# Performance work log

Measured on AMD Instinct MI355X. Metric: run time of the kernel, lower is better.

Reference implementation:

```python
import jax, jax.numpy as jnp
import numpy as np

EPS = 1e-12  # F.normalize default eps


def setup_inputs() -> dict:
    key = jax.random.key(0)
    k1, k2, k3, k4 = jax.random.split(key, 4)
    dim, heads = 192, 6
    B, H, W = 8, 128, 128
    x = jax.random.normal(k1, (B, dim, H, W), dtype=jnp.float32)
    qkv_w = jax.random.normal(k2, (3 * dim, dim), dtype=jnp.float32) * 0.05
    qkv_dw_w = jax.random.normal(k3, (3 * dim, 1, 3, 3), dtype=jnp.float32) * 0.05
    proj_w = jax.random.normal(k4, (dim, dim), dtype=jnp.float32) * 0.05
    temperature = jnp.ones((heads, 1, 1), dtype=jnp.float32)
    return {"x": x, "qkv_w": qkv_w, "qkv_dw_w": qkv_dw_w,
            "proj_w": proj_w, "temperature": temperature}


def _l2norm(t):
    # F.normalize(t, dim=-1): t / max(||t||_2, eps)
    n = jnp.sqrt(jnp.sum(t * t, axis=-1, keepdims=True))
    return t / jnp.maximum(n, EPS)


def reference(x, qkv_w, qkv_dw_w, proj_w, temperature):
    B, C, H, W = x.shape
    heads = temperature.shape[0]
    ch = C // heads  # channels per head

    # 1x1 pointwise conv (no bias)
    qkv = jnp.einsum('oc,bchw->bohw', qkv_w, x)
    # depthwise 3x3 conv, padding=1, groups = 3*C
    qkv = jax.lax.conv_general_dilated(
        qkv, qkv_dw_w, window_strides=(1, 1), padding='SAME',
        feature_group_count=3 * C,
        dimension_numbers=('NCHW', 'OIHW', 'NCHW'))

    q, k, v = jnp.split(qkv, 3, axis=1)
    # b (hd c) h w -> b hd c (h w)
    def split_heads(t):
        return t.reshape(B, heads, ch, H * W)
    q, k, v = split_heads(q), split_heads(k), split_heads(v)

    q = _l2norm(q)
    k = _l2norm(k)

    # channel attention: [b, hd, c, c], contraction over HW
    attn = jnp.einsum('bhcn,bhdn->bhcd', q, k) * temperature[None]
    attn = jax.nn.softmax(attn, axis=-1)

    out = jnp.einsum('bhcd,bhdn->bhcn', attn, v)  # [b, hd, c, HW]
    out = out.reshape(B, C, H, W)
    # final 1x1 projection
    return jnp.einsum('oc,bchw->bohw', proj_w, out)
```

## Files before the change

### kernel.cpp

```cpp
#include <hip/hip_runtime.h>
#include <type_traits>

typedef __attribute__((ext_vector_type(8))) short bf16x8;
typedef __attribute__((ext_vector_type(4))) float f32x4;

#define NB 8
#define NC 192
#define NO 576
#define NHW 16384
#define NH 6

__device__ __forceinline__ float bf2f(unsigned short u){
  return __uint_as_float(((unsigned int)u) << 16);
}
__device__ __forceinline__ unsigned short f2bf(float f){
  unsigned int u = __float_as_uint(f);
  u += 0x7FFFu + ((u >> 16) & 1u);
  return (unsigned short)(u >> 16);
}

__device__ __forceinline__ void st1(unsigned short* p, float v){ *p = f2bf(v); }
__device__ __forceinline__ void st1(float* p, float v){ *p = v; }

#define LSTR 200

__global__ void cvt_w(const float* __restrict__ w, unsigned short* __restrict__ wb, int n4){
  const int i = blockIdx.x*256 + threadIdx.x;
  if (i < n4){
    float4 f = *(const float4*)(w + (long long)i*4);
    *(ushort4*)(wb + (long long)i*4) = make_ushort4(f2bf(f.x), f2bf(f.y), f2bf(f.z), f2bf(f.w));
  }
}

template<typename BT, typename OT>
__global__ __launch_bounds__(256) void gemm192v2(
    const unsigned short* __restrict__ A, long long a_bstride, int o_tiles,
    const BT* __restrict__ Bm, long long b_bstride,
    OT* __restrict__ Out, long long o_bstride)
{
  __shared__ __align__(16) unsigned short Xt[128 * LSTR];
  const int t  = threadIdx.x;
  const int b  = blockIdx.z;
  const int n0 = blockIdx.x * 128;
  const BT* Bb = Bm + b_bstride * b;

  for (int idx = t; idx < 1536; idx += 256){
    const int n4 = (idx & 31) * 4;
    const int c  = (idx >> 5) * 4;
    if constexpr (std::is_same<BT, float>::value){
      float4 f0 = *(const float4*)(Bb + (long long)(c+0)*NHW + n0 + n4);
      float4 f1 = *(const float4*)(Bb + (long long)(c+1)*NHW + n0 + n4);
      float4 f2 = *(const float4*)(Bb + (long long)(c+2)*NHW + n0 + n4);
      float4 f3 = *(const float4*)(Bb + (long long)(c+3)*NHW + n0 + n4);
      *(ushort4*)&Xt[(n4+0)*LSTR + c] = make_ushort4(f2bf(f0.x), f2bf(f1.x), f2bf(f2.x), f2bf(f3.x));
      *(ushort4*)&Xt[(n4+1)*LSTR + c] = make_ushort4(f2bf(f0.y), f2bf(f1.y), f2bf(f2.y), f2bf(f3.y));
      *(ushort4*)&Xt[(n4+2)*LSTR + c] = make_ushort4(f2bf(f0.z), f2bf(f1.z), f2bf(f2.z), f2bf(f3.z));
      *(ushort4*)&Xt[(n4+3)*LSTR + c] = make_ushort4(f2bf(f0.w), f2bf(f1.w), f2bf(f2.w), f2bf(f3.w));
    } else {
      ushort4 u0 = *(const ushort4*)(Bb + (long long)(c+0)*NHW + n0 + n4);
      ushort4 u1 = *(const ushort4*)(Bb + (long long)(c+1)*NHW + n0 + n4);
      ushort4 u2 = *(const ushort4*)(Bb + (long long)(c+2)*NHW + n0 + n4);
      ushort4 u3 = *(const ushort4*)(Bb + (long long)(c+3)*NHW + n0 + n4);
      *(ushort4*)&Xt[(n4+0)*LSTR + c] = make_ushort4(u0.x, u1.x, u2.x, u3.x);
      *(ushort4*)&Xt[(n4+1)*LSTR + c] = make_ushort4(u0.y, u1.y, u2.y, u3.y);
      *(ushort4*)&Xt[(n4+2)*LSTR + c] = make_ushort4(u0.z, u1.z, u2.z, u3.z);
      *(ushort4*)&Xt[(n4+3)*LSTR + c] = make_ushort4(u0.w, u1.w, u2.w, u3.w);
    }
  }
  __syncthreads();

  const int l  = t & 63;
  const int w  = t >> 6;
  const int wo = (w >> 1) * 32;
  const int wn = (w & 1) * 64;
  const int lr = l & 15;
  const int lg = l >> 4;

  const unsigned short* Ab = A + a_bstride * b;
  OT* ob = Out + o_bstride * b;

  for (int ot = 0; ot < o_tiles; ++ot){
    const int o0 = ot * 64;
    const unsigned short* Aw = Ab + (long long)(o0 + wo + lr) * NC;

    f32x4 acc[2][4];
    #pragma unroll
    for (int i=0;i<2;i++)
      #pragma unroll
      for (int j=0;j<4;j++) acc[i][j] = (f32x4){0.f,0.f,0.f,0.f};

    #pragma unroll
    for (int k = 0; k < 192; k += 32){
      const int kc = k + lg*8;
      bf16x8 a0 = *(const bf16x8*)(Aw + kc);
      bf16x8 a1 = *(const bf16x8*)(Aw + 16*NC + kc);
      bf16x8 b0 = *(const bf16x8*)&Xt[(wn +      lr)*LSTR + kc];
      bf16x8 b1 = *(const bf16x8*)&Xt[(wn + 16 + lr)*LSTR + kc];
      bf16x8 b2 = *(const bf16x8*)&Xt[(wn + 32 + lr)*LSTR + kc];
      bf16x8 b3 = *(const bf16x8*)&Xt[(wn + 48 + lr)*LSTR + kc];
      acc[0][0] = __builtin_amdgcn_mfma_f32_16x16x32_bf16(a0, b0, acc[0][0], 0,0,0);
      acc[0][1] = __builtin_amdgcn_mfma_f32_16x16x32_bf16(a0, b1, acc[0][1], 0,0,0);
      acc[0][2] = __builtin_amdgcn_mfma_f32_16x16x32_bf16(a0, b2, acc[0][2], 0,0,0);
      acc[0][3] = __builtin_amdgcn_mfma_f32_16x16x32_bf16(a0, b3, acc[0][3], 0,0,0);
      acc[1][0] = __builtin_amdgcn_mfma_f32_16x16x32_bf16(a1, b0, acc[1][0], 0,0,0);
      acc[1][1] = __builtin_amdgcn_mfma_f32_16x16x32_bf16(a1, b1, acc[1][1], 0,0,0);
      acc[1][2] = __builtin_amdgcn_mfma_f32_16x16x32_bf16(a1, b2, acc[1][2], 0,0,0);
      acc[1][3] = __builtin_amdgcn_mfma_f32_16x16x32_bf16(a1, b3, acc[1][3], 0,0,0);
    }

    #pragma unroll
    for (int i=0;i<2;i++)
      #pragma unroll
      for (int j=0;j<4;j++)
        #pragma unroll
        for (int r=0;r<4;r++){
          const int oo = o0 + wo + i*16 + lg*4 + r;
          const int nn = n0 + wn + j*16 + lr;
          st1(ob + (long long)oo*NHW + nn, acc[i][j][r]);
        }
  }
}

__global__ __launch_bounds__(256) void dwconv(const unsigned short* __restrict__ pw,
    const float* __restrict__ wdw, unsigned short* __restrict__ outp,
    float* __restrict__ sumsq)
{
  const int b  = blockIdx.z;
  const int ch = blockIdx.y;
  const int t  = threadIdx.x;
  const int y  = blockIdx.x * 8 + (t >> 5);
  const int x0 = (t & 31) * 4;
  const unsigned short* base = pw + (((long long)b*NO + ch) << 14);
  float w[9];
  #pragma unroll
  for (int i=0;i<9;i++) w[i] = wdw[ch*9 + i];

  float acc0=0.f, acc1=0.f, acc2=0.f, acc3=0.f;
  #pragma unroll
  for (int dy=-1; dy<=1; dy++){
    const int yy = y + dy;
    if (yy < 0 || yy > 127) continue;
    const unsigned short* rp = base + (yy << 7);
    ushort4 v = *(const ushort4*)(rp + x0);
    const float a0 = bf2f(v.x), a1 = bf2f(v.y), a2 = bf2f(v.z), a3 = bf2f(v.w);
    const float aL = (x0 > 0)   ? bf2f(rp[x0-1]) : 0.f;
    const float aR = (x0 < 124) ? bf2f(rp[x0+4]) : 0.f;
    const float w0 = w[(dy+1)*3], w1 = w[(dy+1)*3+1], w2 = w[(dy+1)*3+2];
    acc0 += w0*aL + w1*a0 + w2*a1;
    acc1 += w0*a0 + w1*a1 + w2*a2;
    acc2 += w0*a1 + w1*a2 + w2*a3;
    acc3 += w0*a2 + w1*a3 + w2*aR;
  }
  const unsigned short r0=f2bf(acc0), r1=f2bf(acc1), r2=f2bf(acc2), r3=f2bf(acc3);
  *(ushort4*)(outp + (((long long)b*NO + ch) << 14) + (y << 7) + x0) = make_ushort4(r0,r1,r2,r3);

  if (ch < 384){
    const float f0=bf2f(r0), f1=bf2f(r1), f2v=bf2f(r2), f3=bf2f(r3);
    float s = f0*f0 + f1*f1 + f2v*f2v + f3*f3;
    #pragma unroll
    for (int off=32; off; off>>=1) s += __shfl_down(s, off);
    __shared__ float red[4];
    if ((t & 63) == 0) red[t >> 6] = s;
    __syncthreads();
    if (t == 0) atomicAdd(&sumsq[b*384 + ch], red[0]+red[1]+red[2]+red[3]);
  }
}

__global__ __launch_bounds__(256) void qkdots(const unsigned short* __restrict__ dw,
                                              float* __restrict__ partial)
{
  const int bh = blockIdx.x, ns = blockIdx.y;
  const int b = bh / 6, h = bh - b*6;
  const int t = threadIdx.x, w = t >> 6, l = t & 63, lr = l & 15, lg = l >> 4;
  const unsigned short* qb = dw + ((long long)b*NO + h*32) * NHW;
  const unsigned short* kb = dw + ((long long)b*NO + 192 + h*32) * NHW;
  const int nb = ns*1024 + w*256;
  f32x4 acc00 = {0.f,0.f,0.f,0.f}, acc01 = {0.f,0.f,0.f,0.f};
  f32x4 acc10 = {0.f,0.f,0.f,0.f}, acc11 = {0.f,0.f,0.f,0.f};
  #pragma unroll
  for (int kk=0; kk<8; kk++){
    const int n = nb + kk*32 + lg*8;
    bf16x8 a0 = *(const bf16x8*)(qb + (long long)(     lr)*NHW + n);
    bf16x8 a1 = *(const bf16x8*)(qb + (long long)(16 + lr)*NHW + n);
    bf16x8 b0 = *(const bf16x8*)(kb + (long long)(     lr)*NHW + n);
    bf16x8 b1 = *(const bf16x8*)(kb + (long long)(16 + lr)*NHW + n);
    acc00 = __builtin_amdgcn_mfma_f32_16x16x32_bf16(a0, b0, acc00, 0,0,0);
    acc01 = __builtin_amdgcn_mfma_f32_16x16x32_bf16(a0, b1, acc01, 0,0,0);
    acc10 = __builtin_amdgcn_mfma_f32_16x16x32_bf16(a1, b0, acc10, 0,0,0);
    acc11 = __builtin_amdgcn_mfma_f32_16x16x32_bf16(a1, b1, acc11, 0,0,0);
  }
  __shared__ float pl[4][32][32];
  #pragma unroll
  for (int r=0;r<4;r++){
    pl[w][ 0 + lg*4 + r][ 0 + lr] = acc00[r];
    pl[w][ 0 + lg*4 + r][16 + lr] = acc01[r];
    pl[w][16 + lg*4 + r][ 0 + lr] = acc10[r];
    pl[w][16 + lg*4 + r][16 + lr] = acc11[r];
  }
  __syncthreads();
  for (int e=t; e<1024; e+=256){
    const int r = e >> 5, c = e & 31;
    partial[((long long)bh*16 + ns)*1024 + e] = pl[0][r][c] + pl[1][r][c] + pl[2][r][c] + pl[3][r][c];
  }
}

__global__ __launch_bounds__(256) void softmaxk(const float* __restrict__ partial,
    const float* __restrict__ sumsq, const float* __restrict__ temp,
    float* __restrict__ attn)
{
  const int bh = blockIdx.x, b = bh / 6, h = bh - b*6;
  const int t = threadIdx.x;
  __shared__ float L[32][33];
  for (int e=t; e<1024; e+=256){
    const int c = e >> 5, d = e & 31;
    float s = 0.f;
    #pragma unroll
    for (int i=0;i<16;i++) s += partial[((long long)bh*16 + i)*1024 + e];
    const float nq = fmaxf(sqrtf(sumsq[b*384 + h*32 + c]),        1e-12f);
    const float nk = fmaxf(sqrtf(sumsq[b*384 + 192 + h*32 + d]),  1e-12f);
    L[c][d] = s / (nq * nk) * temp[h];
  }
  __syncthreads();
  if (t < 32){
    float m = -1e30f;
    #pragma unroll
    for (int d=0; d<32; d++) m = fmaxf(m, L[t][d]);
    float e[32]; float sum = 0.f;
    #pragma unroll
    for (int d=0; d<32; d++){ e[d] = expf(L[t][d] - m); sum += e[d]; }
    const float inv = 1.f / sum;
    #pragma unroll
    for (int d=0; d<32; d++) attn[(long long)bh*1024 + t*32 + d] = e[d] * inv;
  }
}

__global__ void mcombk(const float* __restrict__ proj, const float* __restrict__ attn,
                       unsigned short* __restrict__ mc)
{
  const int b = blockIdx.x, o = blockIdx.y, d = threadIdx.x;
  const int h = d >> 5, d32 = d & 31;
  const float* pr = proj + o*NC + h*32;
  const float* at = attn + ((long long)(b*NH + h))*1024 + d32;
  float acc = 0.f;
  #pragma unroll
  for (int c=0;c<32;c++) acc += pr[c] * at[c*32];
  mc[((long long)b*NC + o)*NC + d] = f2bf(acc);
}

extern "C" void kernel_launch(void* const* d_in, const int* in_sizes, int n_in,
                              void* d_out, int out_size, void* d_ws, size_t ws_size,
                              hipStream_t stream) {
  const float* x         = (const float*)d_in[0];
  const float* qkv_w     = (const float*)d_in[1];
  const float* qkv_dw_w  = (const float*)d_in[2];
  const float* proj_w    = (const float*)d_in[3];
  const float* temp      = (const float*)d_in[4];
  float* out = (float*)d_out;

  char* ws = (char*)d_ws;
  const size_t off_pw = 0;
  const size_t off_dw = (size_t)NB*NO*NHW*2;
  const size_t off_ss = off_dw + (size_t)NB*NO*NHW*2;
  const size_t off_pp = off_ss + (size_t)NB*384*4;
  const size_t off_at = off_pp + (size_t)48*16*1024*4;
  const size_t off_mc = off_at + (size_t)48*1024*4;
  const size_t off_wb = off_mc + (size_t)NB*NC*NC*2;

  unsigned short* pw     = (unsigned short*)(ws + off_pw);
  unsigned short* dwp    = (unsigned short*)(ws + off_dw);
  float*          sumsq  = (float*)(ws + off_ss);
  float*          partial= (float*)(ws + off_pp);
  float*          attn   = (float*)(ws + off_at);
  unsigned short* mcomb  = (unsigned short*)(ws + off_mc);
  unsigned short* wb     = (unsigned short*)(ws + off_wb);

  hipMemsetAsync(sumsq, 0, (size_t)NB*384*sizeof(float), stream);

  cvt_w<<<dim3((NO*NC/4 + 255)/256), 256, 0, stream>>>(qkv_w, wb, NO*NC/4);

  gemm192v2<float, unsigned short><<<dim3(128,1,NB), 256, 0, stream>>>(
      wb, 0LL, 9, x, (long long)NC*NHW, pw, (long long)NO*NHW);

  dwconv<<<dim3(16, NO, NB), 256, 0, stream>>>(pw, qkv_dw_w, dwp, sumsq);

  qkdots<<<dim3(48,16), 256, 0, stream>>>(dwp, partial);

  softmaxk<<<48, 256, 0, stream>>>(partial, sumsq, temp, attn);

  mcombk<<<dim3(NB,192), 192, 0, stream>>>(proj_w, attn, mcomb);

  gemm192v2<unsigned short, float><<<dim3(128,1,NB), 256, 0, stream>>>(
      mcomb, (long long)NC*NC, 3, dwp + (long long)384*NHW, (long long)NO*NHW,
      out, (long long)NC*NHW);
}
```

Baseline: 426.9 us.

## Rewrite depthwise conv with per-thread 8x8 tiles and rolling row window

Each thread now computes an 8x8 output tile by streaming 10 input rows with a rolling three-row accumulator, fetching horizontal halo values via wavefront shuffles instead of extra scalar loads. One block covers a whole channel, cutting redundant input reads and block count. The sum-of-squares reduction drops the LDS/syncthreads step and issues one atomic per wavefront. Fewer, larger blocks (4608) may reduce latency hiding, and the norm now uses unrounded fp32 values.

Measured after the change: 363.3 us. 1.18x faster.

```diff
diff --git a/kernel.cpp b/kernel.cpp
--- a/kernel.cpp
+++ b/kernel.cpp
@@ -121,48 +121,79 @@
   }
 }
 
-__global__ __launch_bounds__(256) void dwconv(const unsigned short* __restrict__ pw,
+__global__ __launch_bounds__(256) void dwconv2(const unsigned short* __restrict__ pw,
     const float* __restrict__ wdw, unsigned short* __restrict__ outp,
     float* __restrict__ sumsq)
 {
-  const int b  = blockIdx.z;
-  const int ch = blockIdx.y;
+  const int ch = blockIdx.x;
+  const int b  = blockIdx.y;
   const int t  = threadIdx.x;
-  const int y  = blockIdx.x * 8 + (t >> 5);
-  const int x0 = (t & 31) * 4;
-  const unsigned short* base = pw + (((long long)b*NO + ch) << 14);
+  const int lane  = t & 63;
+  const int strip = t & 15;
+  const int y0    = (t >> 4) * 8;
+  const int x0    = strip * 8;
+
+  const long long choff = ((long long)b*NO + ch) << 14;
+  const unsigned short* base = pw + choff;
+  unsigned short* ob = outp + choff;
+
   float w[9];
   #pragma unroll
   for (int i=0;i<9;i++) w[i] = wdw[ch*9 + i];
 
-  float acc0=0.f, acc1=0.f, acc2=0.f, acc3=0.f;
-  #pragma unroll
-  for (int dy=-1; dy<=1; dy++){
-    const int yy = y + dy;
-    if (yy < 0 || yy > 127) continue;
-    const unsigned short* rp = base + (yy << 7);
-    ushort4 v = *(const ushort4*)(rp + x0);
-    const float a0 = bf2f(v.x), a1 = bf2f(v.y), a2 = bf2f(v.z), a3 = bf2f(v.w);
-    const float aL = (x0 > 0)   ? bf2f(rp[x0-1]) : 0.f;
-    const float aR = (x0 < 124) ? bf2f(rp[x0+4]) : 0.f;
-    const float w0 = w[(dy+1)*3], w1 = w[(dy+1)*3+1], w2 = w[(dy+1)*3+2];
-    acc0 += w0*aL + w1*a0 + w2*a1;
-    acc1 += w0*a0 + w1*a1 + w2*a2;
-    acc2 += w0*a1 + w1*a2 + w2*a3;
-    acc3 += w0*a2 + w1*a3 + w2*aR;
-  }
-  const unsigned short r0=f2bf(acc0), r1=f2bf(acc1), r2=f2bf(acc2), r3=f2bf(acc3);
-  *(ushort4*)(outp + (((long long)b*NO + ch) << 14) + (y << 7) + x0) = make_ushort4(r0,r1,r2,r3);
+  float a0[8], a1[8], a2[8];
+  #pragma unroll
+  for (int i=0;i<8;i++){ a0[i]=0.f; a1[i]=0.f; a2[i]=0.f; }
+  float ss = 0.f;
+
+  #pragma unroll
+  for (int r = 0; r < 10; ++r){
+    const int yy = y0 - 1 + r;
+    float f[8];
+    if (yy >= 0 && yy <= 127){
+      uint4 u = *(const uint4*)(base + (yy << 7) + x0);
+      f[0]=bf2f((unsigned short)(u.x&0xffff)); f[1]=bf2f((unsigned short)(u.x>>16));
+      f[2]=bf2f((unsigned short)(u.y&0xffff)); f[3]=bf2f((unsigned short)(u.y>>16));
+      f[4]=bf2f((unsigned short)(u.z&0xffff)); f[5]=bf2f((unsigned short)(u.z>>16));
+      f[6]=bf2f((unsigned short)(u.w&0xffff)); f[7]=bf2f((unsigned short)(u.w>>16));
+    } else {
+      #pragma unroll
+      for (int i=0;i<8;i++) f[i]=0.f;
+    }
+    float lf = __shfl(f[7], lane - 1, 64);
+    float rf = __shfl(f[0], lane + 1, 64);
+    if (strip == 0)  lf = 0.f;
+    if (strip == 15) rf = 0.f;
+
+    #pragma unroll
+    for (int i=0;i<8;i++){
+      const float hL = (i==0) ? lf : f[i-1];
+      const float hC = f[i];
+      const float hR = (i==7) ? rf : f[i+1];
+      a0[i] += w[6]*hL + w[7]*hC + w[8]*hR;
+      a1[i] += w[3]*hL + w[4]*hC + w[5]*hR;
+      a2[i] += w[0]*hL + w[1]*hC + w[2]*hR;
+    }
+
+    if (r >= 2){
+      const int yo = y0 + r - 2;
+      uint4 o;
+      o.x = (unsigned int)f2bf(a0[0]) | ((unsigned int)f2bf(a0[1]) << 16);
+      o.y = (unsigned int)f2bf(a0[2]) | ((unsigned int)f2bf(a0[3]) << 16);
+      o.z = (unsigned int)f2bf(a0[4]) | ((unsigned int)f2bf(a0[5]) << 16);
+      o.w = (unsigned int)f2bf(a0[6]) | ((unsigned int)f2bf(a0[7]) << 16);
+      *(uint4*)(ob + (yo << 7) + x0) = o;
+      #pragma unroll
+      for (int i=0;i<8;i++) ss += a0[i]*a0[i];
+    }
+    #pragma unroll
+    for (int i=0;i<8;i++){ a0[i]=a1[i]; a1[i]=a2[i]; a2[i]=0.f; }
+  }
 
   if (ch < 384){
-    const float f0=bf2f(r0), f1=bf2f(r1), f2v=bf2f(r2), f3=bf2f(r3);
-    float s = f0*f0 + f1*f1 + f2v*f2v + f3*f3;
-    #pragma unroll
-    for (int off=32; off; off>>=1) s += __shfl_down(s, off);
-    __shared__ float red[4];
-    if ((t & 63) == 0) red[t >> 6] = s;
-    __syncthreads();
-    if (t == 0) atomicAdd(&sumsq[b*384 + ch], red[0]+red[1]+red[2]+red[3]);
+    #pragma unroll
+    for (int off=32; off; off>>=1) ss += __shfl_down(ss, off);
+    if (lane == 0) atomicAdd(&sumsq[b*384 + ch], ss);
   }
 }
 
@@ -281,7 +312,7 @@
   gemm192v2<float, unsigned short><<<dim3(128,1,NB), 256, 0, stream>>>(
       wb, 0LL, 9, x, (long long)NC*NHW, pw, (long long)NO*NHW);
 
-  dwconv<<<dim3(16, NO, NB), 256, 0, stream>>>(pw, qkv_dw_w, dwp, sumsq);
+  dwconv2<<<dim3(NO, NB), 256, 0, stream>>>(pw, qkv_dw_w, dwp, sumsq);
 
   qkdots<<<dim3(48,16), 256, 0, stream>>>(dwp, partial);
 
```
